# Kernel tuning notes

Hardware: AMD Instinct MI355X
Metric: run time of the kernel (lower is better)

## Reference

```python
import jax, jax.numpy as jnp
import numpy as np
import math

N_EMBD = 1024
HIDDEN = 4 * N_EMBD
N_EXPERTS = 8
TOP_K = 2
B, T = 4, 2048


def new_gelu(x):
    c = math.sqrt(2.0 / math.pi)
    return 0.5 * x * (1.0 + jnp.tanh(c * (x + 0.044715 * x * x * x)))


def setup_inputs() -> dict:
    key = jax.random.key(0)
    ks = jax.random.split(key, 10)
    s = 0.02
    return {
        "x": jax.random.normal(ks[0], (B, T, N_EMBD), dtype=jnp.float32),
        # shared expert (1 shared expert)
        "Wfc_s": jax.random.normal(ks[1], (N_EMBD, HIDDEN), dtype=jnp.float32) * s,
        "bfc_s": jnp.zeros((HIDDEN,), dtype=jnp.float32),
        "Wproj_s": jax.random.normal(ks[2], (HIDDEN, N_EMBD), dtype=jnp.float32) * s,
        "bproj_s": jnp.zeros((N_EMBD,), dtype=jnp.float32),
        # router (no bias)
        "Wr": jax.random.normal(ks[3], (N_EMBD, N_EXPERTS), dtype=jnp.float32) * s,
        # routed experts, stacked on leading expert dim
        "Wfc": jax.random.normal(ks[4], (N_EXPERTS, N_EMBD, HIDDEN), dtype=jnp.float32) * s,
        "bfc": jnp.zeros((N_EXPERTS, HIDDEN), dtype=jnp.float32),
        "Wproj": jax.random.normal(ks[5], (N_EXPERTS, HIDDEN, N_EMBD), dtype=jnp.float32) * s,
        "bproj": jnp.zeros((N_EXPERTS, N_EMBD), dtype=jnp.float32),
    }


def _moe_forward(x, Wfc_s, bfc_s, Wproj_s, bproj_s, Wr, Wfc, bfc, Wproj, bproj):
    Bb, Tt, C = x.shape
    xf = x.reshape(Bb * Tt, C)  # [N, C]
    N = Bb * Tt

    # shared path (1 shared expert, divided by count == 1)
    shared = new_gelu(xf @ Wfc_s + bfc_s) @ Wproj_s + bproj_s

    # router
    logits = xf @ Wr                              # [N, E]
    probs = jax.nn.softmax(logits, axis=-1)
    topk_p, topk_i = jax.lax.top_k(probs, TOP_K)  # [N, K]
    topk_p = topk_p / jnp.sum(topk_p, axis=-1, keepdims=True)

    # dense combine weights: gate[n, e] = normalized prob if expert e selected else 0
    gate = jnp.zeros((N, N_EXPERTS), dtype=xf.dtype)
    gate = gate.at[jnp.arange(N)[:, None], topk_i].add(topk_p)

    routed = jnp.zeros_like(xf)
    for e in range(N_EXPERTS):  # small fixed loop over experts
        h = new_gelu(xf @ Wfc[e] + bfc[e]) @ Wproj[e] + bproj[e]
        routed = routed + h * gate[:, e:e + 1]

    return (shared + routed).reshape(Bb, Tt, C)


def reference(x, Wfc_s, bfc_s, Wproj_s, bproj_s, Wr, Wfc, bfc, Wproj, bproj):
    return _moe_forward(x, Wfc_s, bfc_s, Wproj_s, bproj_s, Wr, Wfc, bfc, Wproj, bproj)
```

## Files before the change

### kernel.cpp

```cpp
#include <hip/hip_runtime.h>
#include <stdint.h>

#define N_TOK 8192
#define C_DIM 1024
#define H_DIM 4096
#define N_EXP 8

typedef __bf16 bf16x8 __attribute__((ext_vector_type(8)));
typedef float floatx4 __attribute__((ext_vector_type(4)));

__device__ __forceinline__ short f2b(float f) {
    unsigned u = __float_as_uint(f);
    unsigned r = (u + 0x7FFFu + ((u >> 16) & 1u)) >> 16;
    return (short)(r & 0xFFFFu);
}

__device__ __forceinline__ float gelu_fast(float x) {
    const float k1 = -2.3025850929940457f;
    const float a1 = -2.302114597830384f;
    const float a3 = -0.10294096656926834f;
    float x2 = x * x;
    float m = x * (a1 + a3 * x2);
    float e = __builtin_amdgcn_exp2f(m);
    return x * __builtin_amdgcn_rcpf(1.0f + e);
    (void)k1;
}

__device__ __forceinline__ void gl_lds16(const short* g, short* l) {
    __builtin_amdgcn_global_load_lds(
        (const __attribute__((address_space(1))) unsigned int*)g,
        (__attribute__((address_space(3))) unsigned int*)l, 16, 0, 0);
}

__global__ void cast_x_k(const float* __restrict__ in, short* __restrict__ out) {
    int i = (blockIdx.x * 256 + threadIdx.x) * 4;
    float4 v = *(const float4*)(in + i);
    short4 o;
    o.x = f2b(v.x); o.y = f2b(v.y); o.z = f2b(v.z); o.w = f2b(v.w);
    *(short4*)(out + i) = o;
}

__global__ void transpose_cast_k(const float* __restrict__ W, short* __restrict__ WT,
                                 int K, int N) {
    __shared__ float tile[32][33];
    size_t moff = (size_t)blockIdx.z * (size_t)K * (size_t)N;
    int n0 = blockIdx.x * 32, k0 = blockIdx.y * 32;
    int tx = threadIdx.x, ty = threadIdx.y;
#pragma unroll
    for (int j = 0; j < 32; j += 8)
        tile[ty + j][tx] = W[moff + (size_t)(k0 + ty + j) * N + n0 + tx];
    __syncthreads();
#pragma unroll
    for (int j = 0; j < 32; j += 8)
        WT[moff + (size_t)(n0 + ty + j) * K + k0 + tx] = f2b(tile[tx][ty + j]);
}

__global__ void init_shared_k(int* __restrict__ tok_list, float* __restrict__ gate_list,
                              int* __restrict__ counts) {
    int i = blockIdx.x * 256 + threadIdx.x;
    tok_list[8 * N_TOK + i] = i;
    gate_list[8 * N_TOK + i] = 1.0f;
    if (i == 0) counts[8] = N_TOK;
}

__global__ void router_k(const float* __restrict__ x, const float* __restrict__ Wr,
                         int* __restrict__ counts, int* __restrict__ tok_list,
                         float* __restrict__ gate_list, int* __restrict__ ent) {
    int token = blockIdx.x * 4 + (threadIdx.x >> 6);
    int lane = threadIdx.x & 63;
    const float* xr = x + (size_t)token * C_DIM;
    float p[8];
#pragma unroll
    for (int e = 0; e < 8; ++e) p[e] = 0.f;
    for (int jj = 0; jj < 4; ++jj) {
        int c = (jj * 64 + lane) * 4;
        float4 xv = *(const float4*)(xr + c);
        const float* w = Wr + (size_t)c * 8;
        float xs[4] = {xv.x, xv.y, xv.z, xv.w};
#pragma unroll
        for (int q = 0; q < 4; ++q)
#pragma unroll
            for (int e = 0; e < 8; ++e) p[e] += xs[q] * w[q * 8 + e];
    }
#pragma unroll
    for (int e = 0; e < 8; ++e)
#pragma unroll
        for (int off = 32; off > 0; off >>= 1) p[e] += __shfl_down(p[e], off);
    if (lane == 0) {
        float mx = p[0];
#pragma unroll
        for (int e = 1; e < 8; ++e) mx = fmaxf(mx, p[e]);
        float ex[8];
#pragma unroll
        for (int e = 0; e < 8; ++e) ex[e] = __expf(p[e] - mx);
        int i1 = 0;
#pragma unroll
        for (int e = 1; e < 8; ++e) if (ex[e] > ex[i1]) i1 = e;
        int i2 = (i1 == 0) ? 1 : 0;
#pragma unroll
        for (int e = 0; e < 8; ++e) if (e != i1 && ex[e] > ex[i2]) i2 = e;
        float s2 = ex[i1] + ex[i2];
        float g1 = ex[i1] / s2, g2 = ex[i2] / s2;
        int pos1 = atomicAdd(&counts[i1], 1);
        tok_list[i1 * N_TOK + pos1] = token;
        gate_list[i1 * N_TOK + pos1] = g1;
        ent[token * 2] = (i1 << 16) | pos1;
        int pos2 = atomicAdd(&counts[i2], 1);
        tok_list[i2 * N_TOK + pos2] = token;
        gate_list[i2 * N_TOK + pos2] = g2;
        ent[token * 2 + 1] = (i2 << 16) | pos2;
    }
}

__global__ void offsets_k(const int* __restrict__ counts, int* __restrict__ offs) {
    if (threadIdx.x == 0) {
        int a = 0;
        for (int e = 0; e < 9; ++e) { offs[e] = a; a += counts[e]; }
    }
}

#define SWZ(r) (((r) ^ ((r) >> 2)) & 3)
template <bool IS_FC>
__global__ __launch_bounds__(256) void gemm_k(
    const short* __restrict__ Abase, const short* __restrict__ Bbase,
    const float* __restrict__ biasbase, short* __restrict__ Out,
    const int* __restrict__ counts, const int* __restrict__ offs,
    const int* __restrict__ tok_base, const float* __restrict__ gate_base,
    int K, int N) {
    const int e = blockIdx.z;
    const int count = counts[e];
    const int gx = gridDim.x;
    int bid = blockIdx.y * gx + blockIdx.x;
    int s = bid >> 6, w = bid & 63;
    const int mt = ((s & 7) << 3) + (w >> 3);
    const int nt = ((s >> 3) << 3) + (w & 7);
    if (mt * 128 >= count) return;
    const int off = offs[e];
    const int n0 = nt * 128, m0 = mt * 128;
    const short* Bm = Bbase + (size_t)e * (size_t)K * (size_t)N;
    const float* bias = biasbase + (size_t)e * (size_t)N;
    const int tid = threadIdx.x;
    const int wave = tid >> 6, lane = tid & 63;

    __shared__ __align__(16) short smem[8192];
    short* As = smem;
    short* Bs = smem + 4096;

    const int r0 = wave * 32 + (lane >> 2), r1 = r0 + 16;
    const int ca0 = ((lane & 3) ^ SWZ(r0)) * 8;
    const int ca1 = ((lane & 3) ^ SWZ(r1)) * 8;

    int am0 = min(m0 + r0, count - 1), am1 = min(m0 + r1, count - 1);
    size_t ga0, ga1;
    if (IS_FC) {
        const int* list = tok_base + e * N_TOK;
        ga0 = (size_t)list[am0];
        ga1 = (size_t)list[am1];
    } else {
        ga0 = (size_t)(off + am0);
        ga1 = (size_t)(off + am1);
    }
    const short* agp0 = Abase + ga0 * K + ca0;
    const short* agp1 = Abase + ga1 * K + ca1;
    const short* bgp0 = Bm + (size_t)(n0 + r0) * K + ca0;
    const short* bgp1 = Bm + (size_t)(n0 + r1) * K + ca1;
    short* asw0 = &As[(wave * 32) * 32];
    short* asw1 = &As[(wave * 32 + 16) * 32];
    short* bsw0 = &Bs[(wave * 32) * 32];
    short* bsw1 = &Bs[(wave * 32 + 16) * 32];

    const int wm = (wave >> 1) * 64, wn = (wave & 1) * 64;
    const int fr = lane & 15, quad = lane >> 4;
    const short* ard[4];
    const short* brd[4];
#pragma unroll
    for (int i = 0; i < 4; ++i) {
        int ra = wm + i * 16 + fr;
        int rb = wn + i * 16 + fr;
        ard[i] = &As[ra * 32 + ((quad ^ SWZ(ra)) << 3)];
        brd[i] = &Bs[rb * 32 + ((quad ^ SWZ(rb)) << 3)];
    }

    floatx4 acc[4][4];
#pragma unroll
    for (int i = 0; i < 4; ++i)
#pragma unroll
        for (int j = 0; j < 4; ++j) acc[i][j] = (floatx4){0.f, 0.f, 0.f, 0.f};

    const int kIters = K / 32;
    for (int kk = 0; kk < kIters; ++kk) {
        __syncthreads();
        gl_lds16(agp0, asw0);
        gl_lds16(agp1, asw1);
        gl_lds16(bgp0, bsw0);
        gl_lds16(bgp1, bsw1);
        agp0 += 32; agp1 += 32; bgp0 += 32; bgp1 += 32;
        __syncthreads();
        bf16x8 af[4], bfv[4];
#pragma unroll
        for (int i = 0; i < 4; ++i) af[i] = *(const bf16x8*)ard[i];
#pragma unroll
        for (int j = 0; j < 4; ++j) bfv[j] = *(const bf16x8*)brd[j];
#pragma unroll
        for (int i = 0; i < 4; ++i)
#pragma unroll
            for (int j = 0; j < 4; ++j)
                acc[i][j] = __builtin_amdgcn_mfma_f32_16x16x32_bf16(af[i], bfv[j], acc[i][j], 0, 0, 0);
    }

    __syncthreads();
    float bcol[4];
#pragma unroll
    for (int j = 0; j < 4; ++j) bcol[j] = bias[n0 + wn + j * 16 + fr];

    short* slab = smem + wave * 1152;
    const int rr = lane >> 2, cc = lane & 3;
    const int srow_m = m0 + wm + rr;
    short* sw = slab + quad * 288 + fr;
    const short* srd = slab + rr * 72 + cc * 16;

#pragma unroll
    for (int i = 0; i < 4; ++i) {
        float g4[4];
        if (!IS_FC) {
            const float* gl = gate_base + e * N_TOK;
#pragma unroll
            for (int r = 0; r < 4; ++r) g4[r] = gl[min(m0 + wm + i * 16 + quad * 4 + r, count - 1)];
        }
#pragma unroll
        for (int j = 0; j < 4; ++j)
#pragma unroll
            for (int r = 0; r < 4; ++r) {
                float v = acc[i][j][r] + bcol[j];
                if (IS_FC) v = gelu_fast(v); else v *= g4[r];
                sw[r * 72 + j * 16] = f2b(v);
            }
        int m = srow_m + i * 16;
        if (m < count) {
            int4 v0 = *(const int4*)srd;
            int4 v1 = *(const int4*)(srd + 8);
            short* orow = Out + (size_t)(off + m) * (size_t)N + n0 + wn + cc * 16;
            *(int4*)orow = v0;
            *(int4*)(orow + 8) = v1;
        }
        __builtin_amdgcn_s_waitcnt(0);
    }
}

__global__ void combine_k(float* __restrict__ out, const short* __restrict__ routc,
                          const int* __restrict__ ent, const int* __restrict__ offs) {
    int tid = threadIdx.x;
    int t = blockIdx.x * 2 + (tid >> 7);
    int c = (tid & 127) * 8;
    int p0 = ent[t * 2], p1 = ent[t * 2 + 1];
    size_t r0 = (size_t)(offs[p0 >> 16] + (p0 & 0xFFFF)) * 1024 + c;
    size_t r1 = (size_t)(offs[p1 >> 16] + (p1 & 0xFFFF)) * 1024 + c;
    size_t rs = (size_t)(16384 + t) * 1024 + c;
    int4 va = *(const int4*)(routc + rs);
    int4 vb = *(const int4*)(routc + r0);
    int4 vc = *(const int4*)(routc + r1);
    float o[8];
    const int* pa = (const int*)&va;
    const int* pb = (const int*)&vb;
    const int* pc = (const int*)&vc;
#pragma unroll
    for (int q = 0; q < 4; ++q) {
        unsigned a = pa[q], b = pb[q], cw = pc[q];
        o[2 * q] = __uint_as_float(a << 16) + __uint_as_float(b << 16) + __uint_as_float(cw << 16);
        o[2 * q + 1] = __uint_as_float(a & 0xFFFF0000u) + __uint_as_float(b & 0xFFFF0000u) +
                       __uint_as_float(cw & 0xFFFF0000u);
    }
    float* op = out + (size_t)t * 1024 + c;
    *(float4*)op = (float4){o[0], o[1], o[2], o[3]};
    *(float4*)(op + 4) = (float4){o[4], o[5], o[6], o[7]};
}

extern "C" void kernel_launch(void* const* d_in, const int* in_sizes, int n_in,
                              void* d_out, int out_size, void* d_ws, size_t ws_size,
                              hipStream_t stream) {
    const float* x       = (const float*)d_in[0];
    const float* Wfc_s   = (const float*)d_in[1];
    const float* bfc_s   = (const float*)d_in[2];
    const float* Wproj_s = (const float*)d_in[3];
    const float* bproj_s = (const float*)d_in[4];
    const float* Wr      = (const float*)d_in[5];
    const float* Wfc     = (const float*)d_in[6];
    const float* bfc     = (const float*)d_in[7];
    const float* Wproj   = (const float*)d_in[8];
    const float* bproj   = (const float*)d_in[9];
    float* out = (float*)d_out;

    char* p = (char*)d_ws;
    short* xb      = (short*)p; p += (size_t)N_TOK * C_DIM * 2;
    short* WfcT    = (short*)p; p += (size_t)9 * C_DIM * H_DIM * 2;
    short* WprojT  = (short*)p; p += (size_t)9 * C_DIM * H_DIM * 2;
    float* bfc_all = (float*)p; p += (size_t)9 * H_DIM * 4;
    float* bpj_all = (float*)p; p += (size_t)9 * C_DIM * 4;
    short* h       = (short*)p; p += (size_t)24576 * H_DIM * 2;
    short* routc   = (short*)p; p += (size_t)24576 * C_DIM * 2;
    int*   counts  = (int*)p;   p += 128;
    int*   offs    = (int*)p;   p += 128;
    int*   tok_list  = (int*)p;   p += (size_t)9 * N_TOK * 4;
    float* gate_list = (float*)p; p += (size_t)9 * N_TOK * 4;
    int*   ent     = (int*)p;   p += (size_t)N_TOK * 2 * 4;

    hipMemsetAsync(counts, 0, 64, stream);
    cast_x_k<<<8192, 256, 0, stream>>>(x, xb);
    transpose_cast_k<<<dim3(128, 32, 8), dim3(32, 8), 0, stream>>>(Wfc, WfcT, 1024, 4096);
    transpose_cast_k<<<dim3(128, 32, 1), dim3(32, 8), 0, stream>>>(Wfc_s, WfcT + (size_t)8 * C_DIM * H_DIM, 1024, 4096);
    transpose_cast_k<<<dim3(32, 128, 8), dim3(32, 8), 0, stream>>>(Wproj, WprojT, 4096, 1024);
    transpose_cast_k<<<dim3(32, 128, 1), dim3(32, 8), 0, stream>>>(Wproj_s, WprojT + (size_t)8 * C_DIM * H_DIM, 4096, 1024);
    hipMemcpyAsync(bfc_all, bfc, (size_t)8 * H_DIM * 4, hipMemcpyDeviceToDevice, stream);
    hipMemcpyAsync(bfc_all + 8 * H_DIM, bfc_s, (size_t)H_DIM * 4, hipMemcpyDeviceToDevice, stream);
    hipMemcpyAsync(bpj_all, bproj, (size_t)8 * C_DIM * 4, hipMemcpyDeviceToDevice, stream);
    hipMemcpyAsync(bpj_all + 8 * C_DIM, bproj_s, (size_t)C_DIM * 4, hipMemcpyDeviceToDevice, stream);
    init_shared_k<<<32, 256, 0, stream>>>(tok_list, gate_list, counts);
    router_k<<<2048, 256, 0, stream>>>(x, Wr, counts, tok_list, gate_list, ent);
    offsets_k<<<1, 64, 0, stream>>>(counts, offs);

    gemm_k<true><<<dim3(32, 64, 9), 256, 0, stream>>>(
        xb, WfcT, bfc_all, h, counts, offs, tok_list, nullptr, C_DIM, H_DIM);
    gemm_k<false><<<dim3(8, 64, 9), 256, 0, stream>>>(
        h, WprojT, bpj_all, routc, counts, offs, nullptr, gate_list, H_DIM, C_DIM);
    combine_k<<<4096, 256, 0, stream>>>(out, routc, ent, offs);
}
```

Baseline: 1.274 ms.

## Rewrite grouped GEMM with 256x256 tiles, double-buffered LDS and interleaved prefetch

The expert GEMM kernel moves from 128x128 tiles with 4 waves and a single LDS buffer to 256x256 tiles with 8 waves, K-steps of 64 and a double-buffered 128KB LDS ping-pong. Global-to-LDS loads for the next tile are issued between MFMA phases, with partial vmcnt waits and s_setprio, so memory latency overlaps with compute instead of stalling at each sync. The larger tiles raise data reuse, but the grid gets coarser, which worsens tail quantization when expert token counts are uneven. The 128KB of LDS may also limit how many blocks fit on each CU despite the launch_bounds(512,2) hint.

```diff
diff --git a/kernel.cpp b/kernel.cpp
--- a/kernel.cpp
+++ b/kernel.cpp
@@ -4,7 +4,6 @@
 #define N_TOK 8192
 #define C_DIM 1024
 #define H_DIM 4096
-#define N_EXP 8
 
 typedef __bf16 bf16x8 __attribute__((ext_vector_type(8)));
 typedef float floatx4 __attribute__((ext_vector_type(4)));
@@ -16,14 +15,12 @@
 }
 
 __device__ __forceinline__ float gelu_fast(float x) {
-    const float k1 = -2.3025850929940457f;
     const float a1 = -2.302114597830384f;
     const float a3 = -0.10294096656926834f;
     float x2 = x * x;
     float m = x * (a1 + a3 * x2);
     float e = __builtin_amdgcn_exp2f(m);
     return x * __builtin_amdgcn_rcpf(1.0f + e);
-    (void)k1;
 }
 
 __device__ __forceinline__ void gl_lds16(const short* g, short* l) {
@@ -120,37 +117,110 @@
 }
 
 #define SWZ(r) (((r) ^ ((r) >> 2)) & 3)
+
+template <bool STAGE>
+__device__ __forceinline__ void tile_body(
+    char* cb, char* sb, int wave,
+    const short* a0, const short* a1, const short* b0, const short* b1, int ko,
+    const int (&aoff)[8], const int (&boff)[4], floatx4 (&acc)[8][4]) {
+    bf16x8 afr[4], bfr[4];
+#pragma unroll
+    for (int n = 0; n < 4; ++n) bfr[n] = *(const bf16x8*)(cb + 32768 + boff[n]);
+#pragma unroll
+    for (int m = 0; m < 4; ++m) afr[m] = *(const bf16x8*)(cb + aoff[m]);
+    if (STAGE) {
+        gl_lds16(a0 + ko, (short*)(sb + wave * 1024));
+        gl_lds16(a1 + ko, (short*)(sb + 8192 + wave * 1024));
+    }
+    __builtin_amdgcn_s_barrier();
+    asm volatile("s_waitcnt lgkmcnt(0)" ::: "memory");
+    __builtin_amdgcn_s_setprio(1);
+#pragma unroll
+    for (int m = 0; m < 4; ++m)
+#pragma unroll
+        for (int n = 0; n < 4; ++n)
+            acc[m][n] = __builtin_amdgcn_mfma_f32_16x16x32_bf16(afr[m], bfr[n], acc[m][n], 0, 0, 0);
+    __builtin_amdgcn_s_setprio(0);
+    __builtin_amdgcn_s_barrier();
+#pragma unroll
+    for (int m = 0; m < 4; ++m) afr[m] = *(const bf16x8*)(cb + aoff[4 + m]);
+    if (STAGE) {
+        gl_lds16(b0 + ko, (short*)(sb + 32768 + wave * 1024));
+        gl_lds16(b1 + ko, (short*)(sb + 40960 + wave * 1024));
+    }
+    __builtin_amdgcn_s_barrier();
+    asm volatile("s_waitcnt lgkmcnt(0)" ::: "memory");
+    __builtin_amdgcn_s_setprio(1);
+#pragma unroll
+    for (int m = 0; m < 4; ++m)
+#pragma unroll
+        for (int n = 0; n < 4; ++n)
+            acc[4 + m][n] = __builtin_amdgcn_mfma_f32_16x16x32_bf16(afr[m], bfr[n], acc[4 + m][n], 0, 0, 0);
+    __builtin_amdgcn_s_setprio(0);
+    if (STAGE) asm volatile("s_waitcnt vmcnt(4)\n\ts_barrier" ::: "memory");
+    else       asm volatile("s_waitcnt vmcnt(0)\n\ts_barrier" ::: "memory");
+#pragma unroll
+    for (int n = 0; n < 4; ++n) bfr[n] = *(const bf16x8*)(cb + 49152 + boff[n]);
+#pragma unroll
+    for (int m = 0; m < 4; ++m) afr[m] = *(const bf16x8*)(cb + 16384 + aoff[m]);
+    if (STAGE) {
+        gl_lds16(a0 + ko + 32, (short*)(sb + 16384 + wave * 1024));
+        gl_lds16(a1 + ko + 32, (short*)(sb + 24576 + wave * 1024));
+    }
+    __builtin_amdgcn_s_barrier();
+    asm volatile("s_waitcnt lgkmcnt(0)" ::: "memory");
+    __builtin_amdgcn_s_setprio(1);
+#pragma unroll
+    for (int m = 0; m < 4; ++m)
+#pragma unroll
+        for (int n = 0; n < 4; ++n)
+            acc[m][n] = __builtin_amdgcn_mfma_f32_16x16x32_bf16(afr[m], bfr[n], acc[m][n], 0, 0, 0);
+    __builtin_amdgcn_s_setprio(0);
+    __builtin_amdgcn_s_barrier();
+#pragma unroll
+    for (int m = 0; m < 4; ++m) afr[m] = *(const bf16x8*)(cb + 16384 + aoff[4 + m]);
+    if (STAGE) {
+        gl_lds16(b0 + ko + 32, (short*)(sb + 49152 + wave * 1024));
+        gl_lds16(b1 + ko + 32, (short*)(sb + 57344 + wave * 1024));
+    }
+    __builtin_amdgcn_s_barrier();
+    asm volatile("s_waitcnt lgkmcnt(0)" ::: "memory");
+    __builtin_amdgcn_s_setprio(1);
+#pragma unroll
+    for (int m = 0; m < 4; ++m)
+#pragma unroll
+        for (int n = 0; n < 4; ++n)
+            acc[4 + m][n] = __builtin_amdgcn_mfma_f32_16x16x32_bf16(afr[m], bfr[n], acc[4 + m][n], 0, 0, 0);
+    __builtin_amdgcn_s_setprio(0);
+    if (STAGE) asm volatile("s_waitcnt vmcnt(4)\n\ts_barrier" ::: "memory");
+    else       __builtin_amdgcn_s_barrier();
+}
+
 template <bool IS_FC>
-__global__ __launch_bounds__(256) void gemm_k(
+__global__ __launch_bounds__(512, 2) void gemm_k(
     const short* __restrict__ Abase, const short* __restrict__ Bbase,
     const float* __restrict__ biasbase, short* __restrict__ Out,
     const int* __restrict__ counts, const int* __restrict__ offs,
     const int* __restrict__ tok_base, const float* __restrict__ gate_base,
     int K, int N) {
+    __shared__ __align__(16) char sm_b[131072];
     const int e = blockIdx.z;
     const int count = counts[e];
-    const int gx = gridDim.x;
-    int bid = blockIdx.y * gx + blockIdx.x;
-    int s = bid >> 6, w = bid & 63;
-    const int mt = ((s & 7) << 3) + (w >> 3);
-    const int nt = ((s >> 3) << 3) + (w & 7);
-    if (mt * 128 >= count) return;
+    const int mt = blockIdx.y, nt = blockIdx.x;
+    if (mt * 256 >= count) return;
     const int off = offs[e];
-    const int n0 = nt * 128, m0 = mt * 128;
+    const int m0 = mt * 256, n0 = nt * 256;
     const short* Bm = Bbase + (size_t)e * (size_t)K * (size_t)N;
     const float* bias = biasbase + (size_t)e * (size_t)N;
     const int tid = threadIdx.x;
     const int wave = tid >> 6, lane = tid & 63;
-
-    __shared__ __align__(16) short smem[8192];
-    short* As = smem;
-    short* Bs = smem + 4096;
-
-    const int r0 = wave * 32 + (lane >> 2), r1 = r0 + 16;
-    const int ca0 = ((lane & 3) ^ SWZ(r0)) * 8;
-    const int ca1 = ((lane & 3) ^ SWZ(r1)) * 8;
-
-    int am0 = min(m0 + r0, count - 1), am1 = min(m0 + r1, count - 1);
+    const int wm128 = (wave >> 2) * 128, wn64 = (wave & 3) * 64;
+    const int fr = lane & 15, quad = lane >> 4;
+
+    const int rs0 = wave * 16 + (lane >> 2), rs1 = 128 + rs0;
+    const int ca0 = ((lane & 3) ^ SWZ(rs0)) * 8;
+    const int ca1 = ((lane & 3) ^ SWZ(rs1)) * 8;
+    int am0 = min(m0 + rs0, count - 1), am1 = min(m0 + rs1, count - 1);
     size_t ga0, ga1;
     if (IS_FC) {
         const int* list = tok_base + e * N_TOK;
@@ -160,72 +230,66 @@
         ga0 = (size_t)(off + am0);
         ga1 = (size_t)(off + am1);
     }
-    const short* agp0 = Abase + ga0 * K + ca0;
-    const short* agp1 = Abase + ga1 * K + ca1;
-    const short* bgp0 = Bm + (size_t)(n0 + r0) * K + ca0;
-    const short* bgp1 = Bm + (size_t)(n0 + r1) * K + ca1;
-    short* asw0 = &As[(wave * 32) * 32];
-    short* asw1 = &As[(wave * 32 + 16) * 32];
-    short* bsw0 = &Bs[(wave * 32) * 32];
-    short* bsw1 = &Bs[(wave * 32 + 16) * 32];
-
-    const int wm = (wave >> 1) * 64, wn = (wave & 1) * 64;
-    const int fr = lane & 15, quad = lane >> 4;
-    const short* ard[4];
-    const short* brd[4];
-#pragma unroll
-    for (int i = 0; i < 4; ++i) {
-        int ra = wm + i * 16 + fr;
-        int rb = wn + i * 16 + fr;
-        ard[i] = &As[ra * 32 + ((quad ^ SWZ(ra)) << 3)];
-        brd[i] = &Bs[rb * 32 + ((quad ^ SWZ(rb)) << 3)];
-    }
-
-    floatx4 acc[4][4];
-#pragma unroll
-    for (int i = 0; i < 4; ++i)
+    const short* a0 = Abase + ga0 * K + ca0;
+    const short* a1 = Abase + ga1 * K + ca1;
+    const short* b0 = Bm + (size_t)(n0 + rs0) * K + ca0;
+    const short* b1 = Bm + (size_t)(n0 + rs1) * K + ca1;
+
+    int aoff[8], boff[4];
+#pragma unroll
+    for (int m = 0; m < 8; ++m) {
+        int r = wm128 + m * 16 + fr;
+        aoff[m] = r * 64 + ((quad ^ SWZ(r)) << 4);
+    }
+#pragma unroll
+    for (int n = 0; n < 4; ++n) {
+        int r = wn64 + n * 16 + fr;
+        boff[n] = r * 64 + ((quad ^ SWZ(r)) << 4);
+    }
+
+    floatx4 acc[8][4];
+#pragma unroll
+    for (int i = 0; i < 8; ++i)
 #pragma unroll
         for (int j = 0; j < 4; ++j) acc[i][j] = (floatx4){0.f, 0.f, 0.f, 0.f};
 
-    const int kIters = K / 32;
-    for (int kk = 0; kk < kIters; ++kk) {
-        __syncthreads();
-        gl_lds16(agp0, asw0);
-        gl_lds16(agp1, asw1);
-        gl_lds16(bgp0, bsw0);
-        gl_lds16(bgp1, bsw1);
-        agp0 += 32; agp1 += 32; bgp0 += 32; bgp1 += 32;
-        __syncthreads();
-        bf16x8 af[4], bfv[4];
-#pragma unroll
-        for (int i = 0; i < 4; ++i) af[i] = *(const bf16x8*)ard[i];
-#pragma unroll
-        for (int j = 0; j < 4; ++j) bfv[j] = *(const bf16x8*)brd[j];
-#pragma unroll
-        for (int i = 0; i < 4; ++i)
-#pragma unroll
-            for (int j = 0; j < 4; ++j)
-                acc[i][j] = __builtin_amdgcn_mfma_f32_16x16x32_bf16(af[i], bfv[j], acc[i][j], 0, 0, 0);
-    }
-
-    __syncthreads();
+    gl_lds16(a0,      (short*)(sm_b +     0 + wave * 1024));
+    gl_lds16(a1,      (short*)(sm_b +  8192 + wave * 1024));
+    gl_lds16(b0,      (short*)(sm_b + 32768 + wave * 1024));
+    gl_lds16(b1,      (short*)(sm_b + 40960 + wave * 1024));
+    gl_lds16(a0 + 32, (short*)(sm_b + 16384 + wave * 1024));
+    gl_lds16(a1 + 32, (short*)(sm_b + 24576 + wave * 1024));
+    gl_lds16(b0 + 32, (short*)(sm_b + 49152 + wave * 1024));
+    gl_lds16(b1 + 32, (short*)(sm_b + 57344 + wave * 1024));
+    asm volatile("s_waitcnt vmcnt(4)\n\ts_barrier" ::: "memory");
+
+    const int kIters = K / 64;
+    for (int t = 0; t < kIters - 1; ++t) {
+        char* cb = sm_b + (t & 1) * 65536;
+        char* sb = sm_b + ((t & 1) ^ 1) * 65536;
+        tile_body<true>(cb, sb, wave, a0, a1, b0, b1, (t + 1) * 64, aoff, boff, acc);
+    }
+    tile_body<false>(sm_b + ((kIters - 1) & 1) * 65536, sm_b, wave,
+                     a0, a1, b0, b1, 0, aoff, boff, acc);
+
     float bcol[4];
 #pragma unroll
-    for (int j = 0; j < 4; ++j) bcol[j] = bias[n0 + wn + j * 16 + fr];
-
-    short* slab = smem + wave * 1152;
+    for (int j = 0; j < 4; ++j) bcol[j] = bias[n0 + wn64 + j * 16 + fr];
+
+    short* slab = (short*)sm_b + wave * 1152;
     const int rr = lane >> 2, cc = lane & 3;
-    const int srow_m = m0 + wm + rr;
+    const int srow_m = m0 + wm128 + rr;
     short* sw = slab + quad * 288 + fr;
     const short* srd = slab + rr * 72 + cc * 16;
-
-#pragma unroll
-    for (int i = 0; i < 4; ++i) {
+    const float* gl = gate_base + (IS_FC ? 0 : e * N_TOK);
+
+#pragma unroll
+    for (int i = 0; i < 8; ++i) {
         float g4[4];
         if (!IS_FC) {
-            const float* gl = gate_base + e * N_TOK;
-#pragma unroll
-            for (int r = 0; r < 4; ++r) g4[r] = gl[min(m0 + wm + i * 16 + quad * 4 + r, count - 1)];
+#pragma unroll
+            for (int r = 0; r < 4; ++r)
+                g4[r] = gl[min(m0 + wm128 + i * 16 + quad * 4 + r, count - 1)];
         }
 #pragma unroll
         for (int j = 0; j < 4; ++j)
@@ -239,11 +303,11 @@
         if (m < count) {
             int4 v0 = *(const int4*)srd;
             int4 v1 = *(const int4*)(srd + 8);
-            short* orow = Out + (size_t)(off + m) * (size_t)N + n0 + wn + cc * 16;
+            short* orow = Out + (size_t)(off + m) * (size_t)N + n0 + wn64 + cc * 16;
             *(int4*)orow = v0;
             *(int4*)(orow + 8) = v1;
         }
-        __builtin_amdgcn_s_waitcnt(0);
+        asm volatile("s_waitcnt lgkmcnt(0)" ::: "memory");
     }
 }
 
@@ -318,9 +382,9 @@
     router_k<<<2048, 256, 0, stream>>>(x, Wr, counts, tok_list, gate_list, ent);
     offsets_k<<<1, 64, 0, stream>>>(counts, offs);
 
-    gemm_k<true><<<dim3(32, 64, 9), 256, 0, stream>>>(
-        xb, WfcT, bfc_all, h, counts, offs, tok_list, nullptr, C_DIM, H_DIM);
-    gemm_k<false><<<dim3(8, 64, 9), 256, 0, stream>>>(
-        h, WprojT, bpj_all, routc, counts, offs, nullptr, gate_list, H_DIM, C_DIM);
+    gemm_k<true><<<dim3(16, 32, 9), 512, 0, stream>>>(
+        xb, WfcT, bfc_all, h, counts, offs, tok_list, gate_list, C_DIM, H_DIM);
+    gemm_k<false><<<dim3(4, 32, 9), 512, 0, stream>>>(
+        h, WprojT, bpj_all, routc, counts, offs, tok_list, gate_list, H_DIM, C_DIM);
     combine_k<<<4096, 256, 0, stream>>>(out, routc, ent, offs);
 }
```

Result: faster. 1.084 ms (-14.9%).
